# Kernel tuning notes

Measured on AMD Instinct MI355X. Metric: run time of the kernel, lower is better.

## Reference

```python
import jax, jax.numpy as jnp
import numpy as np

B, G, N_IN, N_HID, N_OUT = 2, 4096, 8, 32, 32
ALPHA, BETA, BN_EPS = 0.005, 5e-5, 1e-5
EDGE_P = 0.05  # adjacency density


def _lin_init(k, fan_in, fan_out):
    k1, k2 = jax.random.split(k)
    lim = 1.0 / np.sqrt(fan_in)
    W = jax.random.uniform(k1, (fan_in, fan_out), minval=-lim, maxval=lim, dtype=jnp.float32)
    b = jax.random.uniform(k2, (fan_out,), minval=-lim, maxval=lim, dtype=jnp.float32)
    return W, b


def setup_inputs() -> dict:
    key = jax.random.key(0)
    ks = jax.random.split(key, 12)
    W_infer, b_infer = _lin_init(ks[0], N_IN, N_HID)
    W_e1, b_e1 = _lin_init(ks[1], 2 * N_HID, 1)
    W_e2, b_e2 = _lin_init(ks[2], 2 * N_HID, 1)
    W_n1, b_n1 = _lin_init(ks[3], 2 * N_HID, N_OUT)
    W_n2, b_n2 = _lin_init(ks[4], 2 * N_HID, N_OUT)
    W_m1, b_m1 = _lin_init(ks[5], 2 * N_HID, N_OUT)
    W_m2, b_m2 = _lin_init(ks[6], 2 * N_HID, N_OUT)
    x = jax.random.normal(ks[7], (B, G, N_IN), dtype=jnp.float32)
    edges1 = jax.random.bernoulli(ks[8], EDGE_P, (G, G)).astype(jnp.float32)
    edges2 = jax.random.bernoulli(ks[9], EDGE_P, (G, G)).astype(jnp.float32)
    bn_gamma = jnp.ones((G,), jnp.float32)
    bn_beta = jnp.zeros((G,), jnp.float32)
    return dict(x=x, edges1=edges1, edges2=edges2, W_infer=W_infer, b_infer=b_infer,
                W_e1=W_e1, b_e1=b_e1, W_e2=W_e2, b_e2=b_e2,
                W_n1=W_n1, b_n1=b_n1, W_n2=W_n2, b_n2=b_n2,
                W_m1=W_m1, b_m1=b_m1, W_m2=W_m2, b_m2=b_m2,
                bn_gamma=bn_gamma, bn_beta=bn_beta)


def _mp_block(x, adj, coef, W_e, b_e, W_n, b_n, W_m, b_m):
    # x: [B,G,H]. Torch builds edge feature at flat index k=i*G+j as cat([x_j, x_i])
    # (shape2 = col gather, shape1 = row gather). We keep the same math without
    # materializing the [B,G*G,2H] tensor.
    Hh = x.shape[-1]
    s_src = x @ W_e[:Hh]   # [B,G,1]  (x_j part of mlp_edge)
    s_dst = x @ W_e[Hh:]   # [B,G,1]  (x_i part of mlp_edge)
    logits = s_dst[:, :, None, 0] + s_src[:, None, :, 0] + b_e[0]   # [B,G,G] at (i,j)
    w = adj + coef * (adj == 0).astype(x.dtype)                     # ori_edge + coef*thres_edge
    e = jax.nn.sigmoid(logits) * w[None]                            # [B,G,G]
    # receive at node i: sum_j e_ij * [x_j, x_i]
    recv_src = jnp.einsum('bij,bjh->bih', e, x)                     # sum_j e_ij x_j
    recv_dst = x * jnp.sum(e, axis=2)[..., None]                    # x_i * sum_j e_ij
    recv = jnp.concatenate([recv_src, recv_dst], axis=-1)           # [B,G,2H]
    recv = jax.nn.elu(recv @ W_n + b_n)                             # nodes_mlp + elu
    upd = jnp.concatenate([recv, x], axis=-1) @ W_m + b_m           # mesg_merge (mode='cat')
    return jax.nn.elu(upd)


def _forward(x, edges1, edges2, W_infer, b_infer, W_e1, b_e1, W_e2, b_e2,
             W_n1, b_n1, W_n2, b_n2, W_m1, b_m1, W_m2, b_m2, bn_gamma, bn_beta):
    h = jax.nn.elu(x @ W_infer + b_infer)                           # infer + elu, [B,G,H]
    h = _mp_block(h, edges1, ALPHA, W_e1, b_e1, W_n1, b_n1, W_m1, b_m1)
    # BatchNorm1d(gene_num) on [B, G, n_out]: per-gene stats over (batch, feature)
    mu = jnp.mean(h, axis=(0, 2), keepdims=True)
    var = jnp.var(h, axis=(0, 2), keepdims=True)
    h = (h - mu) * jax.lax.rsqrt(var + BN_EPS)
    h = h * bn_gamma[None, :, None] + bn_beta[None, :, None]
    return _mp_block(h, edges2, BETA, W_e2, b_e2, W_n2, b_n2, W_m2, b_m2)


def reference(x, edges1, edges2, W_infer, b_infer, W_e1, b_e1, W_e2, b_e2,
              W_n1, b_n1, W_n2, b_n2, W_m1, b_m1, W_m2, b_m2, bn_gamma, bn_beta):
    return _forward(x, edges1, edges2, W_infer, b_infer, W_e1, b_e1, W_e2, b_e2,
                    W_n1, b_n1, W_n2, b_n2, W_m1, b_m1, W_m2, b_m2, bn_gamma, bn_beta)
```

## Files before the change

### kernel.cpp

```cpp
#include <hip/hip_runtime.h>

#define G 4096
#define BSZ 2
#define NIN 8
#define HID 32

typedef __attribute__((ext_vector_type(8))) short short8;
typedef __attribute__((ext_vector_type(4))) float floatx4;
typedef __attribute__((ext_vector_type(2))) short short2v;
typedef __attribute__((ext_vector_type(4))) short short4v;
typedef unsigned short ushort_t;

__device__ __forceinline__ float elu1(float v) {
    return v > 0.f ? v : (__expf(v) - 1.f);
}
__device__ __forceinline__ ushort_t f2bf(float f) {
    unsigned u = __float_as_uint(f);
    u += 0x7fffu + ((u >> 16) & 1u);
    return (ushort_t)(u >> 16);
}

__global__ void k_setup1(const float* __restrict__ x, const float* __restrict__ W,
                         const float* __restrict__ bias, const float* __restrict__ We,
                         float* __restrict__ h0, ushort_t* __restrict__ hTb,
                         float* __restrict__ ssrc, float* __restrict__ sdst) {
    int t = blockIdx.x * blockDim.x + threadIdx.x;
    if (t >= BSZ * G) return;
    int b = t >> 12, g = t & (G - 1);
    float xin[NIN];
    const float* xp = x + t * NIN;
#pragma unroll
    for (int k = 0; k < NIN; k++) xin[k] = xp[k];
    float ss = 0.f, sd = 0.f;
    float* hp = h0 + (size_t)t * HID;
#pragma unroll
    for (int o = 0; o < HID; o++) {
        float v = bias[o];
#pragma unroll
        for (int k = 0; k < NIN; k++) v += xin[k] * W[k * HID + o];
        v = elu1(v);
        hp[o] = v;
        hTb[(size_t)(b * HID + o) * G + g] = f2bf(v);
        ss += v * We[o];
        sd += v * We[HID + o];
    }
    ssrc[t] = ss;
    sdst[t] = sd;
}

__global__ __launch_bounds__(256) void k_main(
    const float* __restrict__ adj, const float* __restrict__ ssrc,
    const float* __restrict__ sdst, const ushort_t* __restrict__ hTb,
    const float* __restrict__ bep, float coef, float* __restrict__ part,
    int chunk) {
    int tid = threadIdx.x;
    int w = tid >> 6, l = tid & 63;
    int b = w >> 1, ihalf = w & 1;
    int i0 = blockIdx.x * 32;
    int i = i0 + ihalf * 16 + (l & 15);
    int kg = l >> 4;
    int jbase = blockIdx.y * chunk;
    float sd = sdst[b * G + i] + bep[0];
    float wm1 = 1.f - coef;
    const float* adjrow = adj + (size_t)i * G + jbase + kg * 8;
    const float* srow = ssrc + b * G + jbase + kg * 8;
    const ushort_t* hb0 = hTb + (size_t)(b * HID + (l & 15)) * G + jbase + kg * 8;
    const ushort_t* hb1 = hb0 + (size_t)16 * G;
    floatx4 c0 = {0.f, 0.f, 0.f, 0.f}, c1 = {0.f, 0.f, 0.f, 0.f};
    float es = 0.f;
    int iters = chunk >> 5;

    float4 pa0 = *(const float4*)(adjrow);
    float4 pa1 = *(const float4*)(adjrow + 4);
    short8 pb0 = *(const short8*)(const void*)(hb0);
    short8 pb1 = *(const short8*)(const void*)(hb1);

    for (int jc = 0; jc < iters; jc++) {
        float4 a0 = pa0, a1 = pa1;
        short8 bf0 = pb0, bf1 = pb1;
        if (jc + 1 < iters) {
            int o = (jc + 1) * 32;
            pa0 = *(const float4*)(adjrow + o);
            pa1 = *(const float4*)(adjrow + o + 4);
            pb0 = *(const short8*)(const void*)(hb0 + o);
            pb1 = *(const short8*)(const void*)(hb1 + o);
        }
        float4 s0 = *(const float4*)(srow + jc * 32);
        float4 s1 = *(const float4*)(srow + jc * 32 + 4);
        float av[8] = {a0.x, a0.y, a0.z, a0.w, a1.x, a1.y, a1.z, a1.w};
        float sv[8] = {s0.x, s0.y, s0.z, s0.w, s1.x, s1.y, s1.z, s1.w};
        short8 af;
#pragma unroll
        for (int t = 0; t < 8; t++) {
            float wgt = __builtin_fmaf(av[t], wm1, coef);
            float sg = __builtin_amdgcn_rcpf(1.f + __expf(-(sd + sv[t])));
            float e = sg * wgt;
            es += e;
            af[t] = (short)f2bf(e);
        }
        c0 = __builtin_amdgcn_mfma_f32_16x16x32_bf16(af, bf0, c0, 0, 0, 0);
        c1 = __builtin_amdgcn_mfma_f32_16x16x32_bf16(af, bf1, c1, 0, 0, 0);
    }
    es += __shfl_xor(es, 16);
    es += __shfl_xor(es, 32);
    size_t rb = ((size_t)(blockIdx.y * BSZ + b)) * G;
#pragma unroll
    for (int r = 0; r < 4; r++) {
        int row = i0 + ihalf * 16 + kg * 4 + r;
        part[(rb + row) * 33 + (l & 15)] = c0[r];
        part[(rb + row) * 33 + 16 + (l & 15)] = c1[r];
    }
    if (l < 16) part[(rb + i) * 33 + 32] = es;
}

template <bool DO_BN>
__global__ __launch_bounds__(256) void k_post(
    const float* __restrict__ part, const float* __restrict__ hin,
    const float* __restrict__ Wn, const float* __restrict__ bnb,
    const float* __restrict__ Wm, const float* __restrict__ bmb,
    const float* __restrict__ gamma, const float* __restrict__ beta,
    const float* __restrict__ We2, float* __restrict__ outp,
    ushort_t* __restrict__ hTb, float* __restrict__ s2s,
    float* __restrict__ s2d, int jsn) {
    __shared__ float Wns[64 * 32];
    __shared__ float Wms[64 * 32];
    __shared__ float rec[8][68];
    __shared__ float rec2[8][68];
    __shared__ ushort_t tb[BSZ][HID][4];
    int tid = threadIdx.x;
    int rl = tid >> 5, hh = tid & 31;
#pragma unroll
    for (int r = 0; r < 8; r++) {
        Wns[r * 256 + tid] = Wn[r * 256 + tid];
        Wms[r * 256 + tid] = Wm[r * 256 + tid];
    }
    int g0 = blockIdx.x * 4;
    int b = rl & 1;
    int g = g0 + (rl >> 1);
    int rowf = b * G + g;
    float rs = 0.f, es = 0.f;
    for (int js = 0; js < jsn; js++) {
        size_t base = ((size_t)(js * BSZ + b) * G + g) * 33;
        rs += part[base + hh];
        es += part[base + 32];
    }
    float xv = hin[(size_t)rowf * HID + hh];
    rec[rl][hh] = rs;
    rec[rl][32 + hh] = xv * es;
    __syncthreads();
    float v = bnb[hh];
#pragma unroll
    for (int k4 = 0; k4 < 16; k4++) {
        float4 r4 = *(const float4*)&rec[rl][k4 * 4];
        v += r4.x * Wns[(k4 * 4 + 0) * HID + hh];
        v += r4.y * Wns[(k4 * 4 + 1) * HID + hh];
        v += r4.z * Wns[(k4 * 4 + 2) * HID + hh];
        v += r4.w * Wns[(k4 * 4 + 3) * HID + hh];
    }
    v = elu1(v);
    rec2[rl][hh] = v;
    rec2[rl][32 + hh] = xv;
    __syncthreads();
    float u = bmb[hh];
#pragma unroll
    for (int k4 = 0; k4 < 16; k4++) {
        float4 r4 = *(const float4*)&rec2[rl][k4 * 4];
        u += r4.x * Wms[(k4 * 4 + 0) * HID + hh];
        u += r4.y * Wms[(k4 * 4 + 1) * HID + hh];
        u += r4.z * Wms[(k4 * 4 + 2) * HID + hh];
        u += r4.w * Wms[(k4 * 4 + 3) * HID + hh];
    }
    float h1v = elu1(u);
    if (!DO_BN) {
        outp[(size_t)rowf * HID + hh] = h1v;
    } else {
        float s = h1v, sq = h1v * h1v;
#pragma unroll
        for (int m = 32; m; m >>= 1) {
            s += __shfl_xor(s, m);
            sq += __shfl_xor(sq, m);
        }
        float mu = s * (1.f / 64.f);
        float var = sq * (1.f / 64.f) - mu * mu;
        float rstd = rsqrtf(var + 1e-5f);
        float hn = (h1v - mu) * rstd * gamma[g] + beta[g];
        outp[(size_t)rowf * HID + hh] = hn;
        tb[b][hh][rl >> 1] = f2bf(hn);
        float ps = hn * We2[hh], pd = hn * We2[HID + hh];
#pragma unroll
        for (int m = 16; m; m >>= 1) {
            ps += __shfl_xor(ps, m);
            pd += __shfl_xor(pd, m);
        }
        if (hh == 0) {
            s2s[rowf] = ps;
            s2d[rowf] = pd;
        }
        __syncthreads();
        if (tid < 64) {
            int b2 = tid >> 5, c = tid & 31;
            short4v val = *(const short4v*)&tb[b2][c][0];
            *(short4v*)(void*)&hTb[(size_t)(b2 * HID + c) * G + g0] = val;
        }
    }
}

extern "C" void kernel_launch(void* const* d_in, const int* in_sizes, int n_in,
                              void* d_out, int out_size, void* d_ws, size_t ws_size,
                              hipStream_t stream) {
    const float* x      = (const float*)d_in[0];
    const float* edges1 = (const float*)d_in[1];
    const float* edges2 = (const float*)d_in[2];
    const float* W_inf  = (const float*)d_in[3];
    const float* b_inf  = (const float*)d_in[4];
    const float* W_e1   = (const float*)d_in[5];
    const float* b_e1   = (const float*)d_in[6];
    const float* W_e2   = (const float*)d_in[7];
    const float* b_e2   = (const float*)d_in[8];
    const float* W_n1   = (const float*)d_in[9];
    const float* b_n1   = (const float*)d_in[10];
    const float* W_n2   = (const float*)d_in[11];
    const float* b_n2   = (const float*)d_in[12];
    const float* W_m1   = (const float*)d_in[13];
    const float* b_m1   = (const float*)d_in[14];
    const float* W_m2   = (const float*)d_in[15];
    const float* b_m2   = (const float*)d_in[16];
    const float* bn_g   = (const float*)d_in[17];
    const float* bn_b   = (const float*)d_in[18];
    float* out = (float*)d_out;

    float* ws = (float*)d_ws;
    float* h0   = ws;
    float* h1n  = ws + 262144;
    float* s1s  = ws + 524288;
    float* s1d  = ws + 532480;
    float* s2s  = ws + 540672;
    float* s2d  = ws + 548864;
    float* part = ws + 557056;

    int JSN = 16;
    size_t need16 = ((size_t)557056 + (size_t)16 * BSZ * G * 33 + 131072) * 4;
    if (ws_size < need16) JSN = 8;
    int chunk = G / JSN;
    ushort_t* hTb = (ushort_t*)(part + (size_t)JSN * BSZ * G * 33);

    const float ALPHA = 0.005f, BETA = 5e-5f;

    k_setup1<<<32, 256, 0, stream>>>(x, W_inf, b_inf, W_e1, h0, hTb, s1s, s1d);
    k_main<<<dim3(G / 32, JSN), 256, 0, stream>>>(edges1, s1s, s1d, hTb, b_e1, ALPHA,
                                                  part, chunk);
    k_post<true><<<G / 4, 256, 0, stream>>>(part, h0, W_n1, b_n1, W_m1, b_m1,
                                            bn_g, bn_b, W_e2, h1n, hTb, s2s, s2d, JSN);
    k_main<<<dim3(G / 32, JSN), 256, 0, stream>>>(edges2, s2s, s2d, hTb, b_e2, BETA,
                                                  part, chunk);
    k_post<false><<<G / 4, 256, 0, stream>>>(part, h1n, W_n2, b_n2, W_m2, b_m2,
                                             nullptr, nullptr, nullptr, out,
                                             nullptr, nullptr, nullptr, JSN);
}
```

Measured before the change: 265.2 us.

## Deepen k_main prefetch, stage ssrc in LDS, fix JSN, coalesce setup transposes

The main edge-weighted aggregation kernel now prefetches four iterations of adjacency and bf16 feature tiles ahead instead of one, to hide global memory latency. The per-chunk source scores are staged in shared memory, and the kernel gets a launch-bounds occupancy hint. JSN is fixed at 8 with a compile-time chunk size, and the partial-sum layout is changed to row-major with a stride of 36 so k_post reads contiguous memory. k_setup1 transposes through LDS so the bf16 transposed writes are coalesced 16-byte stores. The cost is more registers for the deeper prefetch and fewer j-splits, which means less parallelism in k_main.

```diff
diff --git a/kernel.cpp b/kernel.cpp
--- a/kernel.cpp
+++ b/kernel.cpp
@@ -4,10 +4,12 @@
 #define BSZ 2
 #define NIN 8
 #define HID 32
+#define JSN 8
+#define CHUNK 512
+#define ITERS 16
 
 typedef __attribute__((ext_vector_type(8))) short short8;
 typedef __attribute__((ext_vector_type(4))) float floatx4;
-typedef __attribute__((ext_vector_type(2))) short short2v;
 typedef __attribute__((ext_vector_type(4))) short short4v;
 typedef unsigned short ushort_t;
 
@@ -20,13 +22,16 @@
     return (ushort_t)(u >> 16);
 }
 
-__global__ void k_setup1(const float* __restrict__ x, const float* __restrict__ W,
-                         const float* __restrict__ bias, const float* __restrict__ We,
-                         float* __restrict__ h0, ushort_t* __restrict__ hTb,
-                         float* __restrict__ ssrc, float* __restrict__ sdst) {
-    int t = blockIdx.x * blockDim.x + threadIdx.x;
-    if (t >= BSZ * G) return;
-    int b = t >> 12, g = t & (G - 1);
+__global__ __launch_bounds__(256) void k_setup1(
+    const float* __restrict__ x, const float* __restrict__ W,
+    const float* __restrict__ bias, const float* __restrict__ We,
+    float* __restrict__ h0, ushort_t* __restrict__ hTb,
+    float* __restrict__ ssrc, float* __restrict__ sdst) {
+    __shared__ __align__(16) ushort_t hs[HID][264];
+    int tid = threadIdx.x;
+    int t = blockIdx.x * 256 + tid;
+    int b = t >> 12;
+    int g0 = (blockIdx.x & 15) * 256;
     float xin[NIN];
     const float* xp = x + t * NIN;
 #pragma unroll
@@ -40,77 +45,98 @@
         for (int k = 0; k < NIN; k++) v += xin[k] * W[k * HID + o];
         v = elu1(v);
         hp[o] = v;
-        hTb[(size_t)(b * HID + o) * G + g] = f2bf(v);
+        hs[o][tid] = f2bf(v);
         ss += v * We[o];
         sd += v * We[HID + o];
     }
     ssrc[t] = ss;
     sdst[t] = sd;
-}
-
-__global__ __launch_bounds__(256) void k_main(
+    __syncthreads();
+#pragma unroll
+    for (int p = 0; p < 4; p++) {
+        int row = p * 8 + (tid >> 5);
+        int c = (tid & 31) * 8;
+        short8 v8 = *(const short8*)&hs[row][c];
+        *(short8*)(void*)&hTb[(size_t)(b * HID + row) * G + g0 + c] = v8;
+    }
+}
+
+__global__ __launch_bounds__(256, 4) void k_main(
     const float* __restrict__ adj, const float* __restrict__ ssrc,
     const float* __restrict__ sdst, const ushort_t* __restrict__ hTb,
-    const float* __restrict__ bep, float coef, float* __restrict__ part,
-    int chunk) {
+    const float* __restrict__ bep, float coef, float* __restrict__ part) {
+    __shared__ __align__(16) float ssm[BSZ][CHUNK];
     int tid = threadIdx.x;
     int w = tid >> 6, l = tid & 63;
     int b = w >> 1, ihalf = w & 1;
     int i0 = blockIdx.x * 32;
+    int jbase = blockIdx.y * CHUNK;
+    {
+        int bb = tid >> 7, ix = (tid & 127) * 4;
+        *(float4*)&ssm[bb][ix] = *(const float4*)&ssrc[bb * G + jbase + ix];
+    }
     int i = i0 + ihalf * 16 + (l & 15);
     int kg = l >> 4;
-    int jbase = blockIdx.y * chunk;
     float sd = sdst[b * G + i] + bep[0];
     float wm1 = 1.f - coef;
     const float* adjrow = adj + (size_t)i * G + jbase + kg * 8;
-    const float* srow = ssrc + b * G + jbase + kg * 8;
     const ushort_t* hb0 = hTb + (size_t)(b * HID + (l & 15)) * G + jbase + kg * 8;
     const ushort_t* hb1 = hb0 + (size_t)16 * G;
     floatx4 c0 = {0.f, 0.f, 0.f, 0.f}, c1 = {0.f, 0.f, 0.f, 0.f};
     float es = 0.f;
-    int iters = chunk >> 5;
-
-    float4 pa0 = *(const float4*)(adjrow);
-    float4 pa1 = *(const float4*)(adjrow + 4);
-    short8 pb0 = *(const short8*)(const void*)(hb0);
-    short8 pb1 = *(const short8*)(const void*)(hb1);
-
-    for (int jc = 0; jc < iters; jc++) {
-        float4 a0 = pa0, a1 = pa1;
-        short8 bf0 = pb0, bf1 = pb1;
-        if (jc + 1 < iters) {
-            int o = (jc + 1) * 32;
-            pa0 = *(const float4*)(adjrow + o);
-            pa1 = *(const float4*)(adjrow + o + 4);
-            pb0 = *(const short8*)(const void*)(hb0 + o);
-            pb1 = *(const short8*)(const void*)(hb1 + o);
-        }
-        float4 s0 = *(const float4*)(srow + jc * 32);
-        float4 s1 = *(const float4*)(srow + jc * 32 + 4);
-        float av[8] = {a0.x, a0.y, a0.z, a0.w, a1.x, a1.y, a1.z, a1.w};
-        float sv[8] = {s0.x, s0.y, s0.z, s0.w, s1.x, s1.y, s1.z, s1.w};
-        short8 af;
-#pragma unroll
-        for (int t = 0; t < 8; t++) {
-            float wgt = __builtin_fmaf(av[t], wm1, coef);
-            float sg = __builtin_amdgcn_rcpf(1.f + __expf(-(sd + sv[t])));
-            float e = sg * wgt;
-            es += e;
-            af[t] = (short)f2bf(e);
-        }
-        c0 = __builtin_amdgcn_mfma_f32_16x16x32_bf16(af, bf0, c0, 0, 0, 0);
-        c1 = __builtin_amdgcn_mfma_f32_16x16x32_bf16(af, bf1, c1, 0, 0, 0);
+
+    float4 pa0[4], pa1[4];
+    short8 pb0[4], pb1[4];
+#pragma unroll
+    for (int d = 0; d < 4; d++) {
+        pa0[d] = *(const float4*)(adjrow + d * 32);
+        pa1[d] = *(const float4*)(adjrow + d * 32 + 4);
+        pb0[d] = *(const short8*)(const void*)(hb0 + d * 32);
+        pb1[d] = *(const short8*)(const void*)(hb1 + d * 32);
+    }
+    __syncthreads();
+    const float* svp = &ssm[b][kg * 8];
+
+    for (int jc = 0; jc < ITERS; jc += 4) {
+#pragma unroll
+        for (int d = 0; d < 4; d++) {
+            float4 a0 = pa0[d], a1 = pa1[d];
+            short8 bf0 = pb0[d], bf1 = pb1[d];
+            int nj = jc + 4 + d;
+            if (nj < ITERS) {
+                pa0[d] = *(const float4*)(adjrow + nj * 32);
+                pa1[d] = *(const float4*)(adjrow + nj * 32 + 4);
+                pb0[d] = *(const short8*)(const void*)(hb0 + nj * 32);
+                pb1[d] = *(const short8*)(const void*)(hb1 + nj * 32);
+            }
+            float4 s0 = *(const float4*)&svp[(jc + d) * 32];
+            float4 s1 = *(const float4*)&svp[(jc + d) * 32 + 4];
+            float av[8] = {a0.x, a0.y, a0.z, a0.w, a1.x, a1.y, a1.z, a1.w};
+            float sv[8] = {s0.x, s0.y, s0.z, s0.w, s1.x, s1.y, s1.z, s1.w};
+            short8 af;
+#pragma unroll
+            for (int t = 0; t < 8; t++) {
+                float wgt = __builtin_fmaf(av[t], wm1, coef);
+                float sg = __builtin_amdgcn_rcpf(1.f + __expf(-(sd + sv[t])));
+                float e = sg * wgt;
+                es += e;
+                af[t] = (short)f2bf(e);
+            }
+            c0 = __builtin_amdgcn_mfma_f32_16x16x32_bf16(af, bf0, c0, 0, 0, 0);
+            c1 = __builtin_amdgcn_mfma_f32_16x16x32_bf16(af, bf1, c1, 0, 0, 0);
+        }
     }
     es += __shfl_xor(es, 16);
     es += __shfl_xor(es, 32);
-    size_t rb = ((size_t)(blockIdx.y * BSZ + b)) * G;
+    int jsb = blockIdx.y;
 #pragma unroll
     for (int r = 0; r < 4; r++) {
         int row = i0 + ihalf * 16 + kg * 4 + r;
-        part[(rb + row) * 33 + (l & 15)] = c0[r];
-        part[(rb + row) * 33 + 16 + (l & 15)] = c1[r];
-    }
-    if (l < 16) part[(rb + i) * 33 + 32] = es;
+        size_t base = ((size_t)(b * G + row) * JSN + jsb) * 36;
+        part[base + (l & 15)] = c0[r];
+        part[base + 16 + (l & 15)] = c1[r];
+    }
+    if (l < 16) part[((size_t)(b * G + i) * JSN + jsb) * 36 + 32] = es;
 }
 
 template <bool DO_BN>
@@ -121,7 +147,7 @@
     const float* __restrict__ gamma, const float* __restrict__ beta,
     const float* __restrict__ We2, float* __restrict__ outp,
     ushort_t* __restrict__ hTb, float* __restrict__ s2s,
-    float* __restrict__ s2d, int jsn) {
+    float* __restrict__ s2d) {
     __shared__ float Wns[64 * 32];
     __shared__ float Wms[64 * 32];
     __shared__ float rec[8][68];
@@ -139,10 +165,11 @@
     int g = g0 + (rl >> 1);
     int rowf = b * G + g;
     float rs = 0.f, es = 0.f;
-    for (int js = 0; js < jsn; js++) {
-        size_t base = ((size_t)(js * BSZ + b) * G + g) * 33;
-        rs += part[base + hh];
-        es += part[base + 32];
+    size_t rbase = (size_t)rowf * JSN * 36;
+#pragma unroll
+    for (int js = 0; js < JSN; js++) {
+        rs += part[rbase + js * 36 + hh];
+        es += part[rbase + js * 36 + 32];
     }
     float xv = hin[(size_t)rowf * HID + hh];
     rec[rl][hh] = rs;
@@ -237,23 +264,16 @@
     float* s2s  = ws + 540672;
     float* s2d  = ws + 548864;
     float* part = ws + 557056;
-
-    int JSN = 16;
-    size_t need16 = ((size_t)557056 + (size_t)16 * BSZ * G * 33 + 131072) * 4;
-    if (ws_size < need16) JSN = 8;
-    int chunk = G / JSN;
-    ushort_t* hTb = (ushort_t*)(part + (size_t)JSN * BSZ * G * 33);
+    ushort_t* hTb = (ushort_t*)(part + (size_t)BSZ * G * JSN * 36);
 
     const float ALPHA = 0.005f, BETA = 5e-5f;
 
     k_setup1<<<32, 256, 0, stream>>>(x, W_inf, b_inf, W_e1, h0, hTb, s1s, s1d);
-    k_main<<<dim3(G / 32, JSN), 256, 0, stream>>>(edges1, s1s, s1d, hTb, b_e1, ALPHA,
-                                                  part, chunk);
+    k_main<<<dim3(G / 32, JSN), 256, 0, stream>>>(edges1, s1s, s1d, hTb, b_e1, ALPHA, part);
     k_post<true><<<G / 4, 256, 0, stream>>>(part, h0, W_n1, b_n1, W_m1, b_m1,
-                                            bn_g, bn_b, W_e2, h1n, hTb, s2s, s2d, JSN);
-    k_main<<<dim3(G / 32, JSN), 256, 0, stream>>>(edges2, s2s, s2d, hTb, b_e2, BETA,
-                                                  part, chunk);
+                                            bn_g, bn_b, W_e2, h1n, hTb, s2s, s2d);
+    k_main<<<dim3(G / 32, JSN), 256, 0, stream>>>(edges2, s2s, s2d, hTb, b_e2, BETA, part);
     k_post<false><<<G / 4, 256, 0, stream>>>(part, h1n, W_n2, b_n2, W_m2, b_m2,
                                              nullptr, nullptr, nullptr, out,
-                                             nullptr, nullptr, nullptr, JSN);
-}
+                                             nullptr, nullptr, nullptr);
+}
```

Measured after the change: 299.1 us. +12.8%, slower.
